# Kernel optimization log

Hardware: AMD Instinct MI355X
Metric: run time of the kernel (lower is better)

The kernel has to match this reference:

```python
import jax, jax.numpy as jnp
import numpy as np

NUM_HEADS = 8

def setup_inputs() -> dict:
    key = jax.random.key(0)
    ks = jax.random.split(key, 5)
    B, N, D = 2, 2048, 512
    x = jax.random.normal(ks[0], (B, N, D), dtype=jnp.float32)
    qkv_w = jax.random.normal(ks[1], (3 * D, D), dtype=jnp.float32) * (D ** -0.5)
    qkv_b = jax.random.normal(ks[2], (3 * D,), dtype=jnp.float32) * 0.02
    proj_w = jax.random.normal(ks[3], (D, D), dtype=jnp.float32) * (D ** -0.5)
    proj_b = jax.random.normal(ks[4], (D,), dtype=jnp.float32) * 0.02
    return {"x": x, "qkv_w": qkv_w, "qkv_b": qkv_b, "proj_w": proj_w, "proj_b": proj_b}

def reference(x, qkv_w, qkv_b, proj_w, proj_b):
    B, N, D = x.shape
    H = NUM_HEADS
    hd = D // H
    scale = hd ** -0.5
    # qkv projection: [B,N,3D] -> [B,N,3,H,hd]
    qkv = (jnp.einsum('bnd,ed->bne', x, qkv_w) + qkv_b).reshape(B, N, 3, H, hd)
    q, k, v = qkv[:, :, 0], qkv[:, :, 1], qkv[:, :, 2]
    q = q * scale
    attn = jnp.einsum('bnhd,bmhd->bhnm', q, k)  # [B,H,N,M]
    # L2-normalize each score row before softmax (the custom modification)
    attn = attn / (jnp.linalg.norm(attn, axis=-1, keepdims=True) + 1e-6)
    attn = jax.nn.softmax(attn, axis=-1)
    out = jnp.einsum('bhnm,bmhd->bnhd', attn, v).reshape(B, N, D)
    return jnp.einsum('bnd,ed->bne', out, proj_w) + proj_b
```

## Files before the change

kernel.cpp:

```cpp
#include <hip/hip_runtime.h>
#include <hip/hip_bf16.h>
#include <cstdint>

typedef __attribute__((ext_vector_type(8))) short short8;
typedef __attribute__((ext_vector_type(4))) float floatx4;

__device__ __forceinline__ unsigned short f2bf(float f) {
  union { float f; unsigned int i; } v; v.f = f;
  unsigned int r = v.i + 0x7FFFu + ((v.i >> 16) & 1u);
  return (unsigned short)(r >> 16);
}

__device__ __forceinline__ void async_copy16(const void* g, void* l) {
  __builtin_amdgcn_global_load_lds(
      (const __attribute__((address_space(1))) void*)g,
      (__attribute__((address_space(3))) void*)l, 16, 0, 0);
}

__global__ __launch_bounds__(256) void f32_to_bf16_kernel(
    const float* __restrict__ in, unsigned short* __restrict__ out, int n8) {
  int i = blockIdx.x * blockDim.x + threadIdx.x;
  if (i >= n8) return;
  const float4* p = (const float4*)in + (size_t)i * 2;
  float4 a = p[0], b = p[1];
  short8 r;
  r[0] = (short)f2bf(a.x); r[1] = (short)f2bf(a.y);
  r[2] = (short)f2bf(a.z); r[3] = (short)f2bf(a.w);
  r[4] = (short)f2bf(b.x); r[5] = (short)f2bf(b.y);
  r[6] = (short)f2bf(b.z); r[7] = (short)f2bf(b.w);
  *(short8*)(out + (size_t)i * 8) = r;
}

template <int BM, int BN, typename OutT>
__global__ __launch_bounds__(256) void gemm_tiled_kernel(
    const unsigned short* __restrict__ A, const unsigned short* __restrict__ W,
    const float* __restrict__ bias, OutT* __restrict__ out,
    int M, int N, int K) {
  constexpr int BK = 64;
  constexpr int MI = BM / 32;
  constexpr int NI = BN / 32;
  __shared__ __align__(16) unsigned short As[BM * BK];
  __shared__ __align__(16) unsigned short Ws[BN * BK];

  int tid = threadIdx.x, wave = tid >> 6, lane = tid & 63;
  int l16 = lane & 15, quad = lane >> 4;
  int bm = blockIdx.x, bn = blockIdx.y;
  int wm = (wave & 1) * (BM / 2), wn = (wave >> 1) * (BN / 2);

  floatx4 acc[MI][NI] = {};

  for (int kk = 0; kk < K; kk += BK) {
    __syncthreads();
#pragma unroll
    for (int c = 0; c < MI; c++) {
      int ci = (wave * MI + c) * 64 + lane;
      int row = ci >> 3, col8 = (ci & 7) ^ (row & 7);
      async_copy16(A + (size_t)(bm * BM + row) * K + kk + col8 * 8,
                   As + (size_t)ci * 8);
    }
#pragma unroll
    for (int c = 0; c < NI; c++) {
      int ci = (wave * NI + c) * 64 + lane;
      int row = ci >> 3, col8 = (ci & 7) ^ (row & 7);
      async_copy16(W + (size_t)(bn * BN + row) * K + kk + col8 * 8,
                   Ws + (size_t)ci * 8);
    }
    __syncthreads();

#pragma unroll
    for (int k2 = 0; k2 < 2; k2++) {
      short8 a[MI], w8[NI];
#pragma unroll
      for (int mi = 0; mi < MI; mi++) {
        int row = wm + mi * 16 + l16;
        int slot = ((k2 * 4 + quad) ^ (row & 7));
        a[mi] = *(const short8*)(As + row * 64 + slot * 8);
      }
#pragma unroll
      for (int ni = 0; ni < NI; ni++) {
        int row = wn + ni * 16 + l16;
        int slot = ((k2 * 4 + quad) ^ (row & 7));
        w8[ni] = *(const short8*)(Ws + row * 64 + slot * 8);
      }
#pragma unroll
      for (int mi = 0; mi < MI; mi++)
#pragma unroll
        for (int ni = 0; ni < NI; ni++)
          acc[mi][ni] = __builtin_amdgcn_mfma_f32_16x16x32_bf16(
              a[mi], w8[ni], acc[mi][ni], 0, 0, 0);
    }
  }

#pragma unroll
  for (int ni = 0; ni < NI; ni++) {
    int col = bn * BN + wn + ni * 16 + l16;
    float bb = bias[col];
#pragma unroll
    for (int mi = 0; mi < MI; mi++) {
#pragma unroll
      for (int r = 0; r < 4; r++) {
        int row = bm * BM + wm + mi * 16 + quad * 4 + r;
        float v = acc[mi][ni][r] + bb;
        if constexpr (sizeof(OutT) == 2)
          out[(size_t)row * N + col] = (OutT)f2bf(v);
        else
          out[(size_t)row * N + col] = (OutT)v;
      }
    }
  }
}

__global__ __launch_bounds__(256) void v_transpose_kernel(
    const unsigned short* __restrict__ qkv, unsigned short* __restrict__ vt) {
  __shared__ __align__(16) unsigned short T[64 * 72];
  int nb = blockIdx.x, bh = blockIdx.y;
  int b = bh >> 3, h = bh & 7;
  int t = threadIdx.x;
#pragma unroll
  for (int c = 0; c < 2; c++) {
    int ci = c * 256 + t;
    int row = ci >> 3, ch = ci & 7;
    *(short8*)(T + row * 72 + ch * 8) = *(const short8*)(
        qkv + (size_t)(b * 2048 + nb * 64 + row) * 1536 + 1024 + h * 64 + ch * 8);
  }
  __syncthreads();
  int d = t & 63, nblk = t >> 6;
  short8 v0, v1;
#pragma unroll
  for (int i = 0; i < 8; i++) v0[i] = (short)T[(nblk * 16 + i) * 72 + d];
#pragma unroll
  for (int i = 0; i < 8; i++) v1[i] = (short)T[(nblk * 16 + 8 + i) * 72 + d];
  size_t orow = ((size_t)bh * 64 + d) * 2048 + nb * 64 + nblk * 16;
  *(short8*)(vt + orow) = v0;
  *(short8*)(vt + orow + 8) = v1;
}

__global__ __launch_bounds__(256) void attn_kernel(
    const unsigned short* __restrict__ qkv,
    const unsigned short* __restrict__ vt,
    unsigned short* __restrict__ attn_out) {
  constexpr int NSEQ = 2048, LD = 1536, DM = 512;
  const float scale = 0.125f;

  __shared__ __align__(16) unsigned short Kb[128 * 64];
  __shared__ __align__(16) unsigned short Vtb[64 * 128];
  __shared__ __align__(16) unsigned short Pb[64 * 128];
  __shared__ float Red[4][64];

  int qb = blockIdx.x, h = blockIdx.y, b = blockIdx.z;
  int tid = threadIdx.x, wave = tid >> 6, lane = tid & 63;
  int l16 = lane & 15, quad = lane >> 4;

  const unsigned short* base = qkv + (size_t)b * NSEQ * LD;
  const unsigned short* vbase = vt + (size_t)(b * 8 + h) * 64 * NSEQ;

  short8 aq[4][2];
#pragma unroll
  for (int mi = 0; mi < 4; mi++) {
    const unsigned short* qp =
        base + (size_t)(qb * 64 + mi * 16 + l16) * LD + h * 64;
    aq[mi][0] = *(const short8*)(qp + quad * 8);
    aq[mi][1] = *(const short8*)(qp + 32 + quad * 8);
  }

  float sumsq[4][4] = {};
  for (int mc = 0; mc < NSEQ; mc += 128) {
    __syncthreads();
#pragma unroll
    for (int c = 0; c < 4; c++) {
      int ci = (wave * 4 + c) * 64 + lane;
      int row = ci >> 3, sc = (ci & 7) ^ (row & 7);
      async_copy16(base + (size_t)(mc + row) * LD + 512 + h * 64 + sc * 8,
                   Kb + (size_t)ci * 8);
    }
    __syncthreads();
#pragma unroll
    for (int st = 0; st < 2; st++) {
      floatx4 acc[4] = {};
      int row = wave * 32 + st * 16 + l16;
#pragma unroll
      for (int k2 = 0; k2 < 2; k2++) {
        short8 bk = *(const short8*)(Kb + row * 64 +
                                     (((k2 * 4 + quad) ^ (row & 7)) * 8));
#pragma unroll
        for (int mi = 0; mi < 4; mi++)
          acc[mi] = __builtin_amdgcn_mfma_f32_16x16x32_bf16(aq[mi][k2], bk,
                                                            acc[mi], 0, 0, 0);
      }
#pragma unroll
      for (int mi = 0; mi < 4; mi++)
#pragma unroll
        for (int r = 0; r < 4; r++) sumsq[mi][r] += acc[mi][r] * acc[mi][r];
    }
  }

#pragma unroll
  for (int mi = 0; mi < 4; mi++)
#pragma unroll
    for (int r = 0; r < 4; r++)
#pragma unroll
      for (int m = 1; m <= 8; m <<= 1)
        sumsq[mi][r] += __shfl_xor(sumsq[mi][r], m, 64);
  if (l16 == 0) {
#pragma unroll
    for (int mi = 0; mi < 4; mi++)
#pragma unroll
      for (int r = 0; r < 4; r++)
        Red[wave][mi * 16 + quad * 4 + r] = sumsq[mi][r];
  }
  __syncthreads();
  float invk[4][4];
#pragma unroll
  for (int mi = 0; mi < 4; mi++)
#pragma unroll
    for (int r = 0; r < 4; r++) {
      int q = mi * 16 + quad * 4 + r;
      float tot = Red[0][q] + Red[1][q] + Red[2][q] + Red[3][q];
      invk[mi][r] = scale / (scale * sqrtf(tot) + 1e-6f);
    }

  floatx4 o[4] = {};
  float lsum[4][4] = {};

  for (int mc = 0; mc < NSEQ; mc += 128) {
    __syncthreads();
#pragma unroll
    for (int c = 0; c < 4; c++) {
      int ci = (wave * 4 + c) * 64 + lane;
      int row = ci >> 3, sc = (ci & 7) ^ (row & 7);
      async_copy16(base + (size_t)(mc + row) * LD + 512 + h * 64 + sc * 8,
                   Kb + (size_t)ci * 8);
    }
#pragma unroll
    for (int c = 0; c < 4; c++) {
      int ci = (wave * 4 + c) * 64 + lane;
      int d = ci >> 4, sc = (ci & 15) ^ (d & 15);
      async_copy16(vbase + (size_t)d * NSEQ + mc + sc * 8,
                   Vtb + (size_t)ci * 8);
    }
    __syncthreads();

#pragma unroll
    for (int st = 0; st < 2; st++) {
      floatx4 acc[4] = {};
      int row = wave * 32 + st * 16 + l16;
#pragma unroll
      for (int k2 = 0; k2 < 2; k2++) {
        short8 bk = *(const short8*)(Kb + row * 64 +
                                     (((k2 * 4 + quad) ^ (row & 7)) * 8));
#pragma unroll
        for (int mi = 0; mi < 4; mi++)
          acc[mi] = __builtin_amdgcn_mfma_f32_16x16x32_bf16(aq[mi][k2], bk,
                                                            acc[mi], 0, 0, 0);
      }
      int kvc = wave * 4 + st * 2 + (l16 >> 3);
#pragma unroll
      for (int mi = 0; mi < 4; mi++)
#pragma unroll
        for (int r = 0; r < 4; r++) {
          float p = __expf(acc[mi][r] * invk[mi][r]);
          lsum[mi][r] += p;
          int q = mi * 16 + quad * 4 + r;
          Pb[q * 128 + ((kvc ^ (q & 15)) * 8) + (l16 & 7)] = f2bf(p);
        }
    }
    __syncthreads();

    short8 bv[4];
    int d = wave * 16 + l16;
#pragma unroll
    for (int ks = 0; ks < 4; ks++)
      bv[ks] = *(const short8*)(Vtb + d * 128 + (((ks * 4 + quad) ^ l16) * 8));
#pragma unroll
    for (int mi = 0; mi < 4; mi++) {
#pragma unroll
      for (int ks = 0; ks < 4; ks++) {
        short8 ap = *(const short8*)(Pb + (mi * 16 + l16) * 128 +
                                     (((ks * 4 + quad) ^ l16) * 8));
        o[mi] = __builtin_amdgcn_mfma_f32_16x16x32_bf16(ap, bv[ks], o[mi],
                                                        0, 0, 0);
      }
    }
  }

#pragma unroll
  for (int mi = 0; mi < 4; mi++)
#pragma unroll
    for (int r = 0; r < 4; r++)
#pragma unroll
      for (int m = 1; m <= 8; m <<= 1)
        lsum[mi][r] += __shfl_xor(lsum[mi][r], m, 64);
  __syncthreads();
  if (l16 == 0) {
#pragma unroll
    for (int mi = 0; mi < 4; mi++)
#pragma unroll
      for (int r = 0; r < 4; r++)
        Red[wave][mi * 16 + quad * 4 + r] = lsum[mi][r];
  }
  __syncthreads();

  size_t ob = ((size_t)b * NSEQ + qb * 64) * DM + h * 64 + wave * 16 + l16;
#pragma unroll
  for (int mi = 0; mi < 4; mi++)
#pragma unroll
    for (int r = 0; r < 4; r++) {
      int q = mi * 16 + quad * 4 + r;
      float tot = Red[0][q] + Red[1][q] + Red[2][q] + Red[3][q];
      attn_out[ob + (size_t)q * DM] = f2bf(o[mi][r] / tot);
    }
}

extern "C" void kernel_launch(void* const* d_in, const int* in_sizes, int n_in,
                              void* d_out, int out_size, void* d_ws, size_t ws_size,
                              hipStream_t stream) {
  const float* x = (const float*)d_in[0];
  const float* qkv_w = (const float*)d_in[1];
  const float* qkv_b = (const float*)d_in[2];
  const float* proj_w = (const float*)d_in[3];
  const float* proj_b = (const float*)d_in[4];
  float* out = (float*)d_out;

  unsigned short* xb = (unsigned short*)d_ws;
  unsigned short* qkvw_b = xb + (size_t)4096 * 512;
  unsigned short* projw_b = qkvw_b + (size_t)1536 * 512;
  unsigned short* qkv = projw_b + (size_t)512 * 512;
  unsigned short* attn_out = qkv + (size_t)4096 * 1536;
  unsigned short* vt = attn_out + (size_t)4096 * 512;

  {
    int n8 = (4096 * 512) / 8;
    f32_to_bf16_kernel<<<(n8 + 255) / 256, 256, 0, stream>>>(x, xb, n8);
    n8 = (1536 * 512) / 8;
    f32_to_bf16_kernel<<<(n8 + 255) / 256, 256, 0, stream>>>(qkv_w, qkvw_b, n8);
    n8 = (512 * 512) / 8;
    f32_to_bf16_kernel<<<(n8 + 255) / 256, 256, 0, stream>>>(proj_w, projw_b, n8);
  }
  gemm_tiled_kernel<128, 64, unsigned short>
      <<<dim3(4096 / 128, 1536 / 64), 256, 0, stream>>>(
          xb, qkvw_b, qkv_b, qkv, 4096, 1536, 512);
  v_transpose_kernel<<<dim3(32, 16), 256, 0, stream>>>(qkv, vt);
  attn_kernel<<<dim3(32, 8, 2), 256, 0, stream>>>(qkv, vt, attn_out);
  gemm_tiled_kernel<64, 64, float>
      <<<dim3(4096 / 64, 512 / 64), 256, 0, stream>>>(
          attn_out, projw_b, proj_b, out, 4096, 512, 512);
}
```

Before: 156.0 us.

## Compute score-row norms via K^T K Gram matrix instead of a full QK pass

Replaces the first full QK^T pass, which existed only to get each score row's L2 norm, with an algebraic identity: the squared norm equals q^T G q, where G = K^T K is a per-head 64x64 Gram matrix. G is built by new transpose, partial-Gram and reduce kernels, and the attention kernel then needs only one pass over keys. The attention kernel also drops its LDS staging of K and V in favour of direct global loads, halves the query tile to 32 rows to double the grid, and merges the three conversion launches into one. Risks are lower precision from G being rounded to bf16, possible cancellation in the norm, extra launches, and less latency hiding for the uncached direct global loads.

```diff
diff --git a/kernel.cpp b/kernel.cpp
--- a/kernel.cpp
+++ b/kernel.cpp
@@ -5,6 +5,11 @@
 typedef __attribute__((ext_vector_type(8))) short short8;
 typedef __attribute__((ext_vector_type(4))) float floatx4;
 
+__device__ __forceinline__ float bf2f(unsigned short u) {
+  union { unsigned int i; float f; } v;
+  v.i = ((unsigned int)u) << 16;
+  return v.f;
+}
 __device__ __forceinline__ unsigned short f2bf(float f) {
   union { float f; unsigned int i; } v; v.f = f;
   unsigned int r = v.i + 0x7FFFu + ((v.i >> 16) & 1u);
@@ -17,18 +22,27 @@
       (__attribute__((address_space(3))) void*)l, 16, 0, 0);
 }
 
-__global__ __launch_bounds__(256) void f32_to_bf16_kernel(
-    const float* __restrict__ in, unsigned short* __restrict__ out, int n8) {
-  int i = blockIdx.x * blockDim.x + threadIdx.x;
-  if (i >= n8) return;
-  const float4* p = (const float4*)in + (size_t)i * 2;
+__global__ __launch_bounds__(256) void convert3_kernel(
+    const float* __restrict__ x, const float* __restrict__ w1,
+    const float* __restrict__ w2, unsigned short* __restrict__ xb,
+    unsigned short* __restrict__ w1b, unsigned short* __restrict__ w2b) {
+  constexpr int N0 = 4096 * 512 / 8, N1 = 1536 * 512 / 8, N2 = 512 * 512 / 8;
+  int i = blockIdx.x * 256 + threadIdx.x;
+  const float* src;
+  unsigned short* dst;
+  int off;
+  if (i < N0) { src = x; dst = xb; off = i; }
+  else if (i < N0 + N1) { src = w1; dst = w1b; off = i - N0; }
+  else if (i < N0 + N1 + N2) { src = w2; dst = w2b; off = i - N0 - N1; }
+  else return;
+  const float4* p = (const float4*)src + (size_t)off * 2;
   float4 a = p[0], b = p[1];
   short8 r;
   r[0] = (short)f2bf(a.x); r[1] = (short)f2bf(a.y);
   r[2] = (short)f2bf(a.z); r[3] = (short)f2bf(a.w);
   r[4] = (short)f2bf(b.x); r[5] = (short)f2bf(b.y);
   r[6] = (short)f2bf(b.z); r[7] = (short)f2bf(b.w);
-  *(short8*)(out + (size_t)i * 8) = r;
+  *(short8*)(dst + (size_t)off * 8) = r;
 }
 
 template <int BM, int BN, typename OutT>
@@ -110,9 +124,11 @@
   }
 }
 
-__global__ __launch_bounds__(256) void v_transpose_kernel(
-    const unsigned short* __restrict__ qkv, unsigned short* __restrict__ vt) {
-  __shared__ __align__(16) unsigned short T[64 * 72];
+__global__ __launch_bounds__(256) void kv_transpose_kernel(
+    const unsigned short* __restrict__ qkv, unsigned short* __restrict__ kt,
+    unsigned short* __restrict__ vt) {
+  __shared__ __align__(16) unsigned short TK[64 * 72];
+  __shared__ __align__(16) unsigned short TV[64 * 72];
   int nb = blockIdx.x, bh = blockIdx.y;
   int b = bh >> 3, h = bh & 7;
   int t = threadIdx.x;
@@ -120,32 +136,70 @@
   for (int c = 0; c < 2; c++) {
     int ci = c * 256 + t;
     int row = ci >> 3, ch = ci & 7;
-    *(short8*)(T + row * 72 + ch * 8) = *(const short8*)(
-        qkv + (size_t)(b * 2048 + nb * 64 + row) * 1536 + 1024 + h * 64 + ch * 8);
+    const unsigned short* src =
+        qkv + (size_t)(b * 2048 + nb * 64 + row) * 1536 + h * 64 + ch * 8;
+    *(short8*)(TK + row * 72 + ch * 8) = *(const short8*)(src + 512);
+    *(short8*)(TV + row * 72 + ch * 8) = *(const short8*)(src + 1024);
   }
   __syncthreads();
   int d = t & 63, nblk = t >> 6;
-  short8 v0, v1;
-#pragma unroll
-  for (int i = 0; i < 8; i++) v0[i] = (short)T[(nblk * 16 + i) * 72 + d];
-#pragma unroll
-  for (int i = 0; i < 8; i++) v1[i] = (short)T[(nblk * 16 + 8 + i) * 72 + d];
+  short8 k0, k1, v0, v1;
+#pragma unroll
+  for (int i = 0; i < 8; i++) {
+    k0[i] = (short)TK[(nblk * 16 + i) * 72 + d];
+    k1[i] = (short)TK[(nblk * 16 + 8 + i) * 72 + d];
+    v0[i] = (short)TV[(nblk * 16 + i) * 72 + d];
+    v1[i] = (short)TV[(nblk * 16 + 8 + i) * 72 + d];
+  }
   size_t orow = ((size_t)bh * 64 + d) * 2048 + nb * 64 + nblk * 16;
+  *(short8*)(kt + orow) = k0;
+  *(short8*)(kt + orow + 8) = k1;
   *(short8*)(vt + orow) = v0;
   *(short8*)(vt + orow + 8) = v1;
+}
+
+__global__ __launch_bounds__(256) void g_partial_kernel(
+    const unsigned short* __restrict__ kt, float* __restrict__ gpart) {
+  int bh = blockIdx.x, sl = blockIdx.y;
+  int tid = threadIdx.x, wave = tid >> 6, lane = tid & 63;
+  int l16 = lane & 15, quad = lane >> 4;
+  const unsigned short* kb = kt + (size_t)bh * 64 * 2048;
+
+  floatx4 acc[4] = {};
+  for (int ks = 0; ks < 16; ks++) {
+    int k0 = sl * 512 + ks * 32 + quad * 8;
+    short8 a = *(const short8*)(kb + (size_t)(wave * 16 + l16) * 2048 + k0);
+#pragma unroll
+    for (int dt = 0; dt < 4; dt++) {
+      short8 bb = *(const short8*)(kb + (size_t)(dt * 16 + l16) * 2048 + k0);
+      acc[dt] = __builtin_amdgcn_mfma_f32_16x16x32_bf16(a, bb, acc[dt], 0, 0, 0);
+    }
+  }
+  float* gout = gpart + ((size_t)(bh * 4 + sl)) * 4096;
+#pragma unroll
+  for (int dt = 0; dt < 4; dt++)
+#pragma unroll
+    for (int r = 0; r < 4; r++)
+      gout[(wave * 16 + quad * 4 + r) * 64 + dt * 16 + l16] = acc[dt][r];
+}
+
+__global__ __launch_bounds__(256) void g_reduce_kernel(
+    const float* __restrict__ gpart, unsigned short* __restrict__ gb) {
+  int i = blockIdx.x * 256 + threadIdx.x;
+  int bh = i >> 12, ed = i & 4095;
+  const float* p = gpart + (size_t)(bh * 4) * 4096 + ed;
+  gb[i] = f2bf(p[0] + p[4096] + p[8192] + p[12288]);
 }
 
 __global__ __launch_bounds__(256) void attn_kernel(
     const unsigned short* __restrict__ qkv,
     const unsigned short* __restrict__ vt,
+    const unsigned short* __restrict__ gb,
     unsigned short* __restrict__ attn_out) {
   constexpr int NSEQ = 2048, LD = 1536, DM = 512;
   const float scale = 0.125f;
 
-  __shared__ __align__(16) unsigned short Kb[128 * 64];
-  __shared__ __align__(16) unsigned short Vtb[64 * 128];
-  __shared__ __align__(16) unsigned short Pb[64 * 128];
-  __shared__ float Red[4][64];
+  __shared__ __align__(16) unsigned short Pb[32 * 128];
 
   int qb = blockIdx.x, h = blockIdx.y, b = blockIdx.z;
   int tid = threadIdx.x, wave = tid >> 6, lane = tid & 63;
@@ -154,159 +208,114 @@
   const unsigned short* base = qkv + (size_t)b * NSEQ * LD;
   const unsigned short* vbase = vt + (size_t)(b * 8 + h) * 64 * NSEQ;
 
-  short8 aq[4][2];
-#pragma unroll
-  for (int mi = 0; mi < 4; mi++) {
+  short8 aq[2][2];
+#pragma unroll
+  for (int mi = 0; mi < 2; mi++) {
     const unsigned short* qp =
-        base + (size_t)(qb * 64 + mi * 16 + l16) * LD + h * 64;
+        base + (size_t)(qb * 32 + mi * 16 + l16) * LD + h * 64;
     aq[mi][0] = *(const short8*)(qp + quad * 8);
     aq[mi][1] = *(const short8*)(qp + 32 + quad * 8);
   }
 
-  float sumsq[4][4] = {};
-  for (int mc = 0; mc < NSEQ; mc += 128) {
-    __syncthreads();
-#pragma unroll
-    for (int c = 0; c < 4; c++) {
-      int ci = (wave * 4 + c) * 64 + lane;
-      int row = ci >> 3, sc = (ci & 7) ^ (row & 7);
-      async_copy16(base + (size_t)(mc + row) * LD + 512 + h * 64 + sc * 8,
-                   Kb + (size_t)ci * 8);
-    }
-    __syncthreads();
-#pragma unroll
-    for (int st = 0; st < 2; st++) {
-      floatx4 acc[4] = {};
-      int row = wave * 32 + st * 16 + l16;
-#pragma unroll
-      for (int k2 = 0; k2 < 2; k2++) {
-        short8 bk = *(const short8*)(Kb + row * 64 +
-                                     (((k2 * 4 + quad) ^ (row & 7)) * 8));
-#pragma unroll
-        for (int mi = 0; mi < 4; mi++)
-          acc[mi] = __builtin_amdgcn_mfma_f32_16x16x32_bf16(aq[mi][k2], bk,
-                                                            acc[mi], 0, 0, 0);
-      }
-#pragma unroll
-      for (int mi = 0; mi < 4; mi++)
-#pragma unroll
-        for (int r = 0; r < 4; r++) sumsq[mi][r] += acc[mi][r] * acc[mi][r];
-    }
-  }
-
-#pragma unroll
-  for (int mi = 0; mi < 4; mi++)
-#pragma unroll
-    for (int r = 0; r < 4; r++)
+  const unsigned short* gbh = gb + (size_t)(b * 8 + h) * 4096;
+  float sumsq[2][4] = {};
+#pragma unroll
+  for (int eti = 0; eti < 4; eti++) {
+    floatx4 t[2] = {};
+#pragma unroll
+    for (int k2 = 0; k2 < 2; k2++) {
+      short8 bg = *(const short8*)(gbh + (eti * 16 + l16) * 64 + k2 * 32 + quad * 8);
+#pragma unroll
+      for (int mi = 0; mi < 2; mi++)
+        t[mi] = __builtin_amdgcn_mfma_f32_16x16x32_bf16(aq[mi][k2], bg, t[mi], 0, 0, 0);
+    }
+#pragma unroll
+    for (int mi = 0; mi < 2; mi++)
+#pragma unroll
+      for (int r = 0; r < 4; r++) {
+        float qv = bf2f(base[(size_t)(qb * 32 + mi * 16 + quad * 4 + r) * LD +
+                             h * 64 + eti * 16 + l16]);
+        sumsq[mi][r] += t[mi][r] * qv;
+      }
+  }
+  float invk[2][4];
+#pragma unroll
+  for (int mi = 0; mi < 2; mi++)
+#pragma unroll
+    for (int r = 0; r < 4; r++) {
 #pragma unroll
       for (int m = 1; m <= 8; m <<= 1)
         sumsq[mi][r] += __shfl_xor(sumsq[mi][r], m, 64);
+      invk[mi][r] = scale / (scale * sqrtf(sumsq[mi][r]) + 1e-6f);
+    }
+
+  floatx4 o[2] = {};
+  float lsum[2][4] = {};
+
+  for (int mc = 0; mc < NSEQ; mc += 128) {
+#pragma unroll
+    for (int st = 0; st < 2; st++) {
+      int kvrow = mc + wave * 32 + st * 16 + l16;
+      const unsigned short* kp = base + (size_t)kvrow * LD + 512 + h * 64;
+      floatx4 s[2] = {};
+#pragma unroll
+      for (int k2 = 0; k2 < 2; k2++) {
+        short8 bk = *(const short8*)(kp + k2 * 32 + quad * 8);
+#pragma unroll
+        for (int mi = 0; mi < 2; mi++)
+          s[mi] = __builtin_amdgcn_mfma_f32_16x16x32_bf16(aq[mi][k2], bk, s[mi], 0, 0, 0);
+      }
+      int kvc = wave * 4 + st * 2 + (l16 >> 3);
+#pragma unroll
+      for (int mi = 0; mi < 2; mi++)
+#pragma unroll
+        for (int r = 0; r < 4; r++) {
+          float p = __expf(s[mi][r] * invk[mi][r]);
+          lsum[mi][r] += p;
+          int q = mi * 16 + quad * 4 + r;
+          Pb[q * 128 + ((kvc ^ (q & 15)) << 3) + (l16 & 7)] = f2bf(p);
+        }
+    }
+    __syncthreads();
+
+    const unsigned short* vp = vbase + (size_t)(wave * 16 + l16) * NSEQ + mc;
+#pragma unroll
+    for (int ks = 0; ks < 4; ks++) {
+      short8 bv = *(const short8*)(vp + ks * 32 + quad * 8);
+#pragma unroll
+      for (int mi = 0; mi < 2; mi++) {
+        int q = mi * 16 + l16;
+        short8 ap = *(const short8*)(Pb + q * 128 + (((ks * 4 + quad) ^ (q & 15)) << 3));
+        o[mi] = __builtin_amdgcn_mfma_f32_16x16x32_bf16(ap, bv, o[mi], 0, 0, 0);
+      }
+    }
+    __syncthreads();
+  }
+
+#pragma unroll
+  for (int mi = 0; mi < 2; mi++)
+#pragma unroll
+    for (int r = 0; r < 4; r++)
+#pragma unroll
+      for (int m = 1; m <= 8; m <<= 1)
+        lsum[mi][r] += __shfl_xor(lsum[mi][r], m, 64);
+  float* Red = (float*)Pb;
   if (l16 == 0) {
 #pragma unroll
-    for (int mi = 0; mi < 4; mi++)
+    for (int mi = 0; mi < 2; mi++)
 #pragma unroll
       for (int r = 0; r < 4; r++)
-        Red[wave][mi * 16 + quad * 4 + r] = sumsq[mi][r];
+        Red[wave * 32 + mi * 16 + quad * 4 + r] = lsum[mi][r];
   }
   __syncthreads();
-  float invk[4][4];
-#pragma unroll
-  for (int mi = 0; mi < 4; mi++)
+
+  size_t ob = ((size_t)b * NSEQ + qb * 32) * DM + h * 64 + wave * 16 + l16;
+#pragma unroll
+  for (int mi = 0; mi < 2; mi++)
 #pragma unroll
     for (int r = 0; r < 4; r++) {
       int q = mi * 16 + quad * 4 + r;
-      float tot = Red[0][q] + Red[1][q] + Red[2][q] + Red[3][q];
-      invk[mi][r] = scale / (scale * sqrtf(tot) + 1e-6f);
-    }
-
-  floatx4 o[4] = {};
-  float lsum[4][4] = {};
-
-  for (int mc = 0; mc < NSEQ; mc += 128) {
-    __syncthreads();
-#pragma unroll
-    for (int c = 0; c < 4; c++) {
-      int ci = (wave * 4 + c) * 64 + lane;
-      int row = ci >> 3, sc = (ci & 7) ^ (row & 7);
-      async_copy16(base + (size_t)(mc + row) * LD + 512 + h * 64 + sc * 8,
-                   Kb + (size_t)ci * 8);
-    }
-#pragma unroll
-    for (int c = 0; c < 4; c++) {
-      int ci = (wave * 4 + c) * 64 + lane;
-      int d = ci >> 4, sc = (ci & 15) ^ (d & 15);
-      async_copy16(vbase + (size_t)d * NSEQ + mc + sc * 8,
-                   Vtb + (size_t)ci * 8);
-    }
-    __syncthreads();
-
-#pragma unroll
-    for (int st = 0; st < 2; st++) {
-      floatx4 acc[4] = {};
-      int row = wave * 32 + st * 16 + l16;
-#pragma unroll
-      for (int k2 = 0; k2 < 2; k2++) {
-        short8 bk = *(const short8*)(Kb + row * 64 +
-                                     (((k2 * 4 + quad) ^ (row & 7)) * 8));
-#pragma unroll
-        for (int mi = 0; mi < 4; mi++)
-          acc[mi] = __builtin_amdgcn_mfma_f32_16x16x32_bf16(aq[mi][k2], bk,
-                                                            acc[mi], 0, 0, 0);
-      }
-      int kvc = wave * 4 + st * 2 + (l16 >> 3);
-#pragma unroll
-      for (int mi = 0; mi < 4; mi++)
-#pragma unroll
-        for (int r = 0; r < 4; r++) {
-          float p = __expf(acc[mi][r] * invk[mi][r]);
-          lsum[mi][r] += p;
-          int q = mi * 16 + quad * 4 + r;
-          Pb[q * 128 + ((kvc ^ (q & 15)) * 8) + (l16 & 7)] = f2bf(p);
-        }
-    }
-    __syncthreads();
-
-    short8 bv[4];
-    int d = wave * 16 + l16;
-#pragma unroll
-    for (int ks = 0; ks < 4; ks++)
-      bv[ks] = *(const short8*)(Vtb + d * 128 + (((ks * 4 + quad) ^ l16) * 8));
-#pragma unroll
-    for (int mi = 0; mi < 4; mi++) {
-#pragma unroll
-      for (int ks = 0; ks < 4; ks++) {
-        short8 ap = *(const short8*)(Pb + (mi * 16 + l16) * 128 +
-                                     (((ks * 4 + quad) ^ l16) * 8));
-        o[mi] = __builtin_amdgcn_mfma_f32_16x16x32_bf16(ap, bv[ks], o[mi],
-                                                        0, 0, 0);
-      }
-    }
-  }
-
-#pragma unroll
-  for (int mi = 0; mi < 4; mi++)
-#pragma unroll
-    for (int r = 0; r < 4; r++)
-#pragma unroll
-      for (int m = 1; m <= 8; m <<= 1)
-        lsum[mi][r] += __shfl_xor(lsum[mi][r], m, 64);
-  __syncthreads();
-  if (l16 == 0) {
-#pragma unroll
-    for (int mi = 0; mi < 4; mi++)
-#pragma unroll
-      for (int r = 0; r < 4; r++)
-        Red[wave][mi * 16 + quad * 4 + r] = lsum[mi][r];
-  }
-  __syncthreads();
-
-  size_t ob = ((size_t)b * NSEQ + qb * 64) * DM + h * 64 + wave * 16 + l16;
-#pragma unroll
-  for (int mi = 0; mi < 4; mi++)
-#pragma unroll
-    for (int r = 0; r < 4; r++) {
-      int q = mi * 16 + quad * 4 + r;
-      float tot = Red[0][q] + Red[1][q] + Red[2][q] + Red[3][q];
+      float tot = Red[q] + Red[32 + q] + Red[64 + q] + Red[96 + q];
       attn_out[ob + (size_t)q * DM] = f2bf(o[mi][r] / tot);
     }
 }
@@ -327,20 +336,18 @@
   unsigned short* qkv = projw_b + (size_t)512 * 512;
   unsigned short* attn_out = qkv + (size_t)4096 * 1536;
   unsigned short* vt = attn_out + (size_t)4096 * 512;
-
-  {
-    int n8 = (4096 * 512) / 8;
-    f32_to_bf16_kernel<<<(n8 + 255) / 256, 256, 0, stream>>>(x, xb, n8);
-    n8 = (1536 * 512) / 8;
-    f32_to_bf16_kernel<<<(n8 + 255) / 256, 256, 0, stream>>>(qkv_w, qkvw_b, n8);
-    n8 = (512 * 512) / 8;
-    f32_to_bf16_kernel<<<(n8 + 255) / 256, 256, 0, stream>>>(proj_w, projw_b, n8);
-  }
+  unsigned short* gbuf = vt + (size_t)16 * 64 * 2048;
+  unsigned short* kt = xb;
+  float* gpart = (float*)qkvw_b;
+
+  convert3_kernel<<<1536, 256, 0, stream>>>(x, qkv_w, proj_w, xb, qkvw_b, projw_b);
   gemm_tiled_kernel<128, 64, unsigned short>
       <<<dim3(4096 / 128, 1536 / 64), 256, 0, stream>>>(
           xb, qkvw_b, qkv_b, qkv, 4096, 1536, 512);
-  v_transpose_kernel<<<dim3(32, 16), 256, 0, stream>>>(qkv, vt);
-  attn_kernel<<<dim3(32, 8, 2), 256, 0, stream>>>(qkv, vt, attn_out);
+  kv_transpose_kernel<<<dim3(32, 16), 256, 0, stream>>>(qkv, kt, vt);
+  g_partial_kernel<<<dim3(16, 4), 256, 0, stream>>>(kt, gpart);
+  g_reduce_kernel<<<256, 256, 0, stream>>>(gpart, gbuf);
+  attn_kernel<<<dim3(64, 8, 2), 256, 0, stream>>>(qkv, vt, gbuf, attn_out);
   gemm_tiled_kernel<64, 64, float>
       <<<dim3(4096 / 64, 512 / 64), 256, 0, stream>>>(
           attn_out, projw_b, proj_b, out, 4096, 512, 512);
```

Measured after the change: 178.7 us. 1.15x slower.
